# Kernel optimization log

Hardware: AMD Instinct MI355X
Metric: run time of the kernel (lower is better)

Reference implementation:

```python
import jax, jax.numpy as jnp
import numpy as np

B, S, E, H, D = 2, 2048, 768, 12, 64  # batch, seq, emb_dim, num_heads, encoder_emb_dim
EPS = 1e-5


def setup_inputs() -> dict:
    key = jax.random.key(0)
    ks = jax.random.split(key, 6)
    # kaiming-uniform-ish bound for fan_in=E
    bound = float(np.sqrt(6.0 / E))
    u = lambda k, shp: jax.random.uniform(k, shp, jnp.float32, -bound, bound)
    return {
        "x": jax.random.normal(ks[0], (B, S, E), jnp.float32),
        "ln_w": jnp.ones((E,), jnp.float32),
        "ln_b": jnp.zeros((E,), jnp.float32),
        "wq": u(ks[1], (E, H * D)),
        "bq": jnp.zeros((H * D,), jnp.float32),
        "wk": u(ks[2], (E, H * D)),
        "bk": jnp.zeros((H * D,), jnp.float32),
        "wv": u(ks[3], (E, H * D)),
        "bv": jnp.zeros((H * D,), jnp.float32),
        "wo": u(ks[4], (H * D, E)),
        "bo": jnp.zeros((E,), jnp.float32),
    }


def reference(x, ln_w, ln_b, wq, bq, wk, bk, wv, bv, wo, bo):
    b, s, _ = x.shape
    # LayerNorm (biased variance, eps=1e-5), as torch.nn.LayerNorm
    mu = x.mean(-1, keepdims=True)
    var = ((x - mu) ** 2).mean(-1, keepdims=True)
    xn = (x - mu) * jax.lax.rsqrt(var + EPS) * ln_w + ln_b

    q = (xn @ wq + bq).reshape(b, s, H, D)
    k = (xn @ wk + bk).reshape(b, s, H, D)
    v = (xn @ wv + bv).reshape(b, s, H, D)

    scale = 1.0 / np.sqrt(D).astype(np.float32)
    scores = jnp.einsum("bihd,bjhd->bhij", q, k) * scale  # [B,H,S,S]

    # masking=True, self_attending=True: mask STRICTLY lower triangle with -inf
    # (i.e. each position attends only to itself and FUTURE positions)
    mask = jnp.tril(jnp.ones((s, s), dtype=bool), k=-1)
    scores = jnp.where(mask, -jnp.inf, scores)

    a = jax.nn.softmax(scores, axis=-1)
    h = jnp.einsum("bhij,bjhd->bihd", a, v).reshape(b, s, H * D)
    return h @ wo + bo
```

## Files before the change

### kernel.cpp

```cpp
#include <hip/hip_runtime.h>

typedef __bf16 bf16_t;
typedef __bf16 bf16x8 __attribute__((ext_vector_type(8)));
typedef __bf16 bf16x4 __attribute__((ext_vector_type(4)));
typedef short  s16x4  __attribute__((ext_vector_type(4)));
typedef float  f32x4  __attribute__((ext_vector_type(4)));
typedef unsigned int u32;

#define BB 2
#define SS 2048
#define EE 768
#define HH 12
#define DD 64
#define NROW (BB*SS)

#define GLDS16(gp, lp) __builtin_amdgcn_global_load_lds( \
    (const __attribute__((address_space(1))) u32*)(gp),   \
    (__attribute__((address_space(3))) u32*)(lp), 16, 0, 0)

#if __has_builtin(__builtin_amdgcn_mfma_f32_16x16x16bf16_1k)
#define MFMA16_BUILTIN 1
static __device__ __forceinline__ f32x4 mfma_16x16x16_bf16(bf16x4 a, bf16x4 b, f32x4 c) {
  return __builtin_amdgcn_mfma_f32_16x16x16bf16_1k(
      __builtin_bit_cast(s16x4, a), __builtin_bit_cast(s16x4, b), c, 0, 0, 0);
}
#else
#define MFMA16_BUILTIN 0
static __device__ __forceinline__ f32x4 mfma_16x16x16_bf16(bf16x4 a, bf16x4 b, f32x4 c) {
  asm volatile("v_mfma_f32_16x16x16_bf16 %0, %1, %2, %0" : "+v"(c) : "v"(a), "v"(b));
  return c;
}
#endif

__global__ __launch_bounds__(256) void pack_w_kernel(
    const float* __restrict__ wq, const float* __restrict__ wk,
    const float* __restrict__ wv, const float* __restrict__ wo,
    bf16_t* __restrict__ wt)
{
  __shared__ float tile[64][65];
  const float* src = (blockIdx.z==0)?wq:(blockIdx.z==1)?wk:(blockIdx.z==2)?wv:wo;
  const int k0 = blockIdx.x*64, n0 = blockIdx.y*64;
  const int t = threadIdx.x;
  #pragma unroll
  for (int it=0; it<16; ++it) {
    int idx = it*256+t, r = idx>>6, c = idx&63;
    tile[r][c] = src[(size_t)(k0+r)*EE + n0 + c];
  }
  __syncthreads();
  bf16_t* dst = wt + (size_t)blockIdx.z*EE*EE;
  #pragma unroll
  for (int it=0; it<16; ++it) {
    int idx = it*256+t, r = idx>>6, c = idx&63;
    dst[(size_t)(n0+r)*EE + k0 + c] = (bf16_t)tile[c][r];
  }
}

__global__ __launch_bounds__(256) void ln_kernel(
    const float* __restrict__ x, const float* __restrict__ w,
    const float* __restrict__ bvec, bf16_t* __restrict__ xn)
{
  const int row = blockIdx.x, t = threadIdx.x;
  const float* xr = x + (size_t)row*EE;
  float v0 = xr[t], v1 = xr[t+256], v2 = xr[t+512];
  float s  = v0+v1+v2;
  float ss = v0*v0 + v1*v1 + v2*v2;
  #pragma unroll
  for (int m=1; m<64; m<<=1) { s += __shfl_xor(s,m); ss += __shfl_xor(ss,m); }
  __shared__ float red[2][4];
  const int wid = t>>6, lane = t&63;
  if (lane==0) { red[0][wid]=s; red[1][wid]=ss; }
  __syncthreads();
  s  = red[0][0]+red[0][1]+red[0][2]+red[0][3];
  ss = red[1][0]+red[1][1]+red[1][2]+red[1][3];
  const float mu   = s*(1.0f/EE);
  const float rstd = rsqrtf(ss*(1.0f/EE) - mu*mu + 1e-5f);
  bf16_t* xo = xn + (size_t)row*EE;
  xo[t      ] = (bf16_t)((v0-mu)*rstd*w[t      ] + bvec[t      ]);
  xo[t + 256] = (bf16_t)((v1-mu)*rstd*w[t + 256] + bvec[t + 256]);
  xo[t + 512] = (bf16_t)((v2-mu)*rstd*w[t + 512] + bvec[t + 512]);
}

__global__ __launch_bounds__(256) void gemm_qkv_kernel(
    const bf16_t* __restrict__ xn, const bf16_t* __restrict__ wt,
    const float* __restrict__ bq, const float* __restrict__ bk, const float* __restrict__ bv,
    bf16_t* __restrict__ qb, bf16_t* __restrict__ kb, bf16_t* __restrict__ vb)
{
  __shared__ __align__(16) bf16_t As[2][128][32];
  __shared__ __align__(16) bf16_t Bs[2][128][32];
  const int bm = blockIdx.x, by = blockIdx.y;
  const int mat = by/6, nb = by%6;
  const bf16_t* W = wt + (size_t)mat*EE*EE + (size_t)nb*128*EE;
  const float* bias = (mat==0)?bq:(mat==1)?bk:bv;
  bf16_t* outp = (mat==0)?qb:(mat==1)?kb:vb;
  const int t = threadIdx.x, lane = t&63, wid = t>>6;
  const int wr = wid>>1, wc = wid&1;
  const int lrow = lane&15, lk = lane>>4;
  const bf16_t* Ag = xn + (size_t)bm*128*EE;

  const int srow = t>>2, sp = t&3;
  const int sg = sp ^ ((srow>>1)&3);
  const int pcs = (lrow>>1)&3;

  auto stage = [&](int buf, int k0) {
    const bf16_t* asrc = Ag + (size_t)srow*EE + k0 + sg*8;
    const bf16_t* bsrc = W  + (size_t)srow*EE + k0 + sg*8;
    GLDS16(asrc,                 &As[buf][0][0] + t*8);
    GLDS16(asrc + (size_t)64*EE, &As[buf][0][0] + 2048 + t*8);
    GLDS16(bsrc,                 &Bs[buf][0][0] + t*8);
    GLDS16(bsrc + (size_t)64*EE, &Bs[buf][0][0] + 2048 + t*8);
  };

  f32x4 acc[4][4];
  #pragma unroll
  for (int i=0;i<4;++i)
    #pragma unroll
    for (int j=0;j<4;++j) acc[i][j] = (f32x4){0.f,0.f,0.f,0.f};

  stage(0, 0);
  __syncthreads();
  int cur = 0;
  for (int k0=0; k0<EE; k0+=32) {
    if (k0+32 < EE) stage(cur^1, k0+32);
    bf16x8 af[4], bfv[4];
    #pragma unroll
    for (int mi=0;mi<4;++mi) af[mi]  = *(const bf16x8*)&As[cur][wr*64+mi*16+lrow][(lk^pcs)*8];
    #pragma unroll
    for (int ni=0;ni<4;++ni) bfv[ni] = *(const bf16x8*)&Bs[cur][wc*64+ni*16+lrow][(lk^pcs)*8];
    #pragma unroll
    for (int mi=0;mi<4;++mi)
      #pragma unroll
      for (int ni=0;ni<4;++ni)
        acc[mi][ni] = __builtin_amdgcn_mfma_f32_16x16x32_bf16(af[mi], bfv[ni], acc[mi][ni], 0,0,0);
    __syncthreads();
    cur ^= 1;
  }
  const int m_base = bm*128 + wr*64;
  const int n_base = nb*128 + wc*64;
  #pragma unroll
  for (int ni=0;ni<4;++ni) {
    const int col = n_base + ni*16 + lrow;
    const float bias_v = bias[col];
    #pragma unroll
    for (int mi=0;mi<4;++mi) {
      #pragma unroll
      for (int r=0;r<4;++r) {
        int row = m_base + mi*16 + 4*lk + r;
        outp[(size_t)row*EE + col] = (bf16_t)(acc[mi][ni][r] + bias_v);
      }
    }
  }
}

__global__ __launch_bounds__(256) void vtrans_kernel(
    const bf16_t* __restrict__ v, bf16_t* __restrict__ vt)
{
  __shared__ __align__(16) bf16_t tile[64][72];
  const int j0 = blockIdx.x*64, bh = blockIdx.y;
  const int b = bh/HH, h = bh%HH;
  const int t = threadIdx.x;
  #pragma unroll
  for (int it=0; it<2; ++it) {
    int idx = it*256+t, r = idx>>3, c8 = (idx&7)*8;
    *(bf16x8*)&tile[r][c8] = *(const bf16x8*)(v + (size_t)(b*SS + j0 + r)*EE + h*DD + c8);
  }
  __syncthreads();
  #pragma unroll
  for (int it=0; it<2; ++it) {
    int idx = it*256+t, d = idx>>3, c8 = (idx&7)*8;
    bf16x8 val;
    #pragma unroll
    for (int i=0;i<8;++i) val[i] = tile[c8+i][d];
    *(bf16x8*)(vt + ((size_t)bh*DD + d)*SS + j0 + c8) = val;
  }
}

__global__ __launch_bounds__(256) void attn_kernel(
    const bf16_t* __restrict__ qb, const bf16_t* __restrict__ kb,
    const bf16_t* __restrict__ vt, bf16_t* __restrict__ hb)
{
  __shared__ __align__(16) bf16_t Ks[2][64][64];
  __shared__ __align__(16) bf16_t Vts[2][64][64];

  const int bid = blockIdx.x;
  const int rnd = bid >> 8, g = bid & 255;
  const int item = (rnd == 1) ? (511 - g) : (rnd*256 + g);
  const int qt = item / 24, bh = item % 24;

  const int i0 = qt*64, b = bh/HH, h = bh%HH;
  const int t = threadIdx.x, lane = t&63, wid = t>>6;
  const int lrow = lane&15, lk = lane>>4;

  const int srow = t>>3, sp = t&7;
  const int sgc = sp ^ (srow&7);
  const bf16_t* kbase  = kb + (size_t)b*SS*EE + h*DD;
  const bf16_t* vtbase = vt + (size_t)bh*DD*SS;

  const bf16_t* qrow = qb + (size_t)(b*SS + i0 + wid*16 + lrow)*EE + h*DD;
  const bf16x8 qf0 = *(const bf16x8*)(qrow + lk*8);
  const bf16x8 qf1 = *(const bf16x8*)(qrow + 32 + lk*8);

  f32x4 acc_ot[4];
  #pragma unroll
  for (int i=0;i<4;++i) acc_ot[i] = (f32x4){0.f,0.f,0.f,0.f};
  float lsum = 0.f;
  const int iloc = wid*16 + lrow;
  const int kkey = lrow&7;

  auto stage = [&](int buf, int jt) {
    const int j0v = jt*64;
    const bf16_t* ksrc = kbase  + (size_t)(j0v + srow)*EE + sgc*8;
    const bf16_t* vsrc = vtbase + (size_t)srow*SS + j0v + sgc*8;
    GLDS16(ksrc,                 &Ks[buf][0][0]  + t*8);
    GLDS16(ksrc + (size_t)32*EE, &Ks[buf][0][0]  + 2048 + t*8);
    GLDS16(vsrc,                 &Vts[buf][0][0] + t*8);
    GLDS16(vsrc + (size_t)32*SS, &Vts[buf][0][0] + 2048 + t*8);
  };

#define ATTN_TILE(CUR, MASKED) do {                                          \
    float e[4][4];                                                           \
    _Pragma("unroll")                                                        \
    for (int sj=0;sj<4;++sj) {                                               \
      const bf16_t* krow = &Ks[CUR][sj*16+lrow][0];                          \
      bf16x8 kf0 = *(const bf16x8*)(krow + ((lk^kkey)<<3));                  \
      bf16x8 kf1 = *(const bf16x8*)(krow + (((lk+4)^kkey)<<3));              \
      f32x4 a = (f32x4){0.f,0.f,0.f,0.f};                                    \
      a = __builtin_amdgcn_mfma_f32_16x16x32_bf16(kf0, qf0, a, 0,0,0);       \
      a = __builtin_amdgcn_mfma_f32_16x16x32_bf16(kf1, qf1, a, 0,0,0);       \
      _Pragma("unroll")                                                      \
      for (int r=0;r<4;++r) {                                                \
        float ee = a[r]*0.180336878f - 34.6246784f;                          \
        if (MASKED && (sj*16 + 4*lk + r) < iloc) ee = -1e30f;                \
        e[sj][r] = ee;                                                       \
      }                                                                      \
    }                                                                        \
    bf16x4 pb[4];                                                            \
    _Pragma("unroll")                                                        \
    for (int sj=0;sj<4;++sj)                                                 \
      _Pragma("unroll")                                                      \
      for (int r=0;r<4;++r) {                                                \
        float p = exp2f(e[sj][r]);                                           \
        lsum += p;                                                           \
        pb[sj][r] = (bf16_t)p;                                               \
      }                                                                      \
    _Pragma("unroll")                                                        \
    for (int sd=0;sd<4;++sd) {                                               \
      const bf16_t* vrow = &Vts[CUR][sd*16+lrow][0];                         \
      _Pragma("unroll")                                                      \
      for (int sj=0;sj<4;++sj) {                                             \
        bf16x4 vf = *(const bf16x4*)(vrow + (((2*sj+(lk>>1))^kkey)<<3) + ((lk&1)<<2)); \
        acc_ot[sd] = mfma_16x16x16_bf16(vf, pb[sj], acc_ot[sd]);             \
      }                                                                      \
    }                                                                        \
  } while(0)

  const int ntiles = SS/64 - qt;
  stage(0, qt);
  __syncthreads();
  if (ntiles > 1) stage(1, qt+1);
  ATTN_TILE(0, true);
#if !MFMA16_BUILTIN
  asm volatile("s_nop 7\n\ts_nop 7");
#endif
  __syncthreads();

  int cur = 1;
  for (int it2=1; it2<ntiles; ++it2) {
    if (it2+1 < ntiles) stage(cur^1, qt+it2+1);
    ATTN_TILE(cur, false);
#if !MFMA16_BUILTIN
    asm volatile("s_nop 7\n\ts_nop 7");
#endif
    __syncthreads();
    cur ^= 1;
  }
#undef ATTN_TILE

  lsum += __shfl_xor(lsum, 16);
  lsum += __shfl_xor(lsum, 32);
  const float inv = 1.0f / lsum;

  const int erow = wid*16 + lrow, ekey = erow&7;
  #pragma unroll
  for (int sd=0;sd<4;++sd) {
    bf16x4 ov;
    #pragma unroll
    for (int r=0;r<4;++r) ov[r] = (bf16_t)(acc_ot[sd][r] * inv);
    *(bf16x4*)(&Ks[0][erow][0] + (((2*sd+(lk>>1))^ekey)<<3) + ((lk&1)<<2)) = ov;
  }
  __syncthreads();
  const int rq = wid*16 + (lane>>2), rkey = rq&7, c4 = lane&3;
  bf16x8 o0 = *(const bf16x8*)(&Ks[0][rq][0] + (((2*c4  )^rkey)<<3));
  bf16x8 o1 = *(const bf16x8*)(&Ks[0][rq][0] + (((2*c4+1)^rkey)<<3));
  bf16_t* orow = hb + (size_t)(b*SS + i0 + rq)*EE + h*DD + c4*16;
  *(bf16x8*)orow = o0;
  *(bf16x8*)(orow+8) = o1;
}

__global__ __launch_bounds__(256) void gemm_out_kernel(
    const bf16_t* __restrict__ hbuf, const bf16_t* __restrict__ wto,
    const float* __restrict__ bo, float* __restrict__ out)
{
  __shared__ __align__(16) bf16_t As[2][128][32];
  __shared__ __align__(16) bf16_t Bs[2][128][32];
  const int bm = blockIdx.x, nb = blockIdx.y;
  const bf16_t* W = wto + (size_t)nb*128*EE;
  const int t = threadIdx.x, lane = t&63, wid = t>>6;
  const int wr = wid>>1, wc = wid&1;
  const int lrow = lane&15, lk = lane>>4;
  const bf16_t* Ag = hbuf + (size_t)bm*128*EE;

  const int srow = t>>2, sp = t&3;
  const int sg = sp ^ ((srow>>1)&3);
  const int pcs = (lrow>>1)&3;

  auto stage = [&](int buf, int k0) {
    const bf16_t* asrc = Ag + (size_t)srow*EE + k0 + sg*8;
    const bf16_t* bsrc = W  + (size_t)srow*EE + k0 + sg*8;
    GLDS16(asrc,                 &As[buf][0][0] + t*8);
    GLDS16(asrc + (size_t)64*EE, &As[buf][0][0] + 2048 + t*8);
    GLDS16(bsrc,                 &Bs[buf][0][0] + t*8);
    GLDS16(bsrc + (size_t)64*EE, &Bs[buf][0][0] + 2048 + t*8);
  };

  f32x4 acc[4][4];
  #pragma unroll
  for (int i=0;i<4;++i)
    #pragma unroll
    for (int j=0;j<4;++j) acc[i][j] = (f32x4){0.f,0.f,0.f,0.f};

  stage(0, 0);
  __syncthreads();
  int cur = 0;
  for (int k0=0; k0<EE; k0+=32) {
    if (k0+32 < EE) stage(cur^1, k0+32);
    bf16x8 af[4], bfv[4];
    #pragma unroll
    for (int mi=0;mi<4;++mi) af[mi]  = *(const bf16x8*)&As[cur][wr*64+mi*16+lrow][(lk^pcs)*8];
    #pragma unroll
    for (int ni=0;ni<4;++ni) bfv[ni] = *(const bf16x8*)&Bs[cur][wc*64+ni*16+lrow][(lk^pcs)*8];
    #pragma unroll
    for (int mi=0;mi<4;++mi)
      #pragma unroll
      for (int ni=0;ni<4;++ni)
        acc[mi][ni] = __builtin_amdgcn_mfma_f32_16x16x32_bf16(af[mi], bfv[ni], acc[mi][ni], 0,0,0);
    __syncthreads();
    cur ^= 1;
  }
  const int m_base = bm*128 + wr*64;
  const int n_base = nb*128 + wc*64;
  #pragma unroll
  for (int ni=0;ni<4;++ni) {
    const int col = n_base + ni*16 + lrow;
    const float bias_v = bo[col];
    #pragma unroll
    for (int mi=0;mi<4;++mi) {
      #pragma unroll
      for (int r=0;r<4;++r) {
        int row = m_base + mi*16 + 4*lk + r;
        out[(size_t)row*EE + col] = acc[mi][ni][r] + bias_v;
      }
    }
  }
}

extern "C" void kernel_launch(void* const* d_in, const int* in_sizes, int n_in,
                              void* d_out, int out_size, void* d_ws, size_t ws_size,
                              hipStream_t stream) {
  const float* x    = (const float*)d_in[0];
  const float* ln_w = (const float*)d_in[1];
  const float* ln_b = (const float*)d_in[2];
  const float* wq   = (const float*)d_in[3];
  const float* bq   = (const float*)d_in[4];
  const float* wk   = (const float*)d_in[5];
  const float* bk   = (const float*)d_in[6];
  const float* wv   = (const float*)d_in[7];
  const float* bv   = (const float*)d_in[8];
  const float* wo   = (const float*)d_in[9];
  const float* bo   = (const float*)d_in[10];
  float* out = (float*)d_out;

  char* ws = (char*)d_ws;
  bf16_t* wt  = (bf16_t*)(ws);
  bf16_t* xn  = (bf16_t*)(ws + 4718592);
  bf16_t* qb  = (bf16_t*)(ws + 11010048);
  bf16_t* kb  = (bf16_t*)(ws + 17301504);
  bf16_t* vb  = (bf16_t*)(ws + 23592960);
  bf16_t* vtb = (bf16_t*)(ws + 29884416);
  bf16_t* hb  = (bf16_t*)(ws + 36175872);

  pack_w_kernel  <<<dim3(12,12,4), 256, 0, stream>>>(wq, wk, wv, wo, wt);
  ln_kernel      <<<dim3(NROW),    256, 0, stream>>>(x, ln_w, ln_b, xn);
  gemm_qkv_kernel<<<dim3(32,18),   256, 0, stream>>>(xn, wt, bq, bk, bv, qb, kb, vb);
  vtrans_kernel  <<<dim3(32,24),   256, 0, stream>>>(vb, vtb);
  attn_kernel    <<<dim3(768),     256, 0, stream>>>(qb, kb, vtb, hb);
  gemm_out_kernel<<<dim3(32,6),    256, 0, stream>>>(hb, wt + (size_t)3*EE*EE, bo, out);
}
```

Measured before the change: 95.58 us.

## Split attention KV range into segments with a separate combine kernel

The attention grid is split along the key dimension. Long query tiles get 2 or 3 segments, giving 1512 blocks instead of 768 with better-balanced work per block. Partial unnormalized outputs and row sums go to fp32 workspace, and a new combine kernel sums and normalizes them. This relies on the softmax not subtracting a running max, so partial sums can simply be added. The cost is an extra kernel launch and fp32 partial-result traffic.

```diff
diff --git a/kernel.cpp b/kernel.cpp
--- a/kernel.cpp
+++ b/kernel.cpp
@@ -176,15 +176,23 @@
 
 __global__ __launch_bounds__(256) void attn_kernel(
     const bf16_t* __restrict__ qb, const bf16_t* __restrict__ kb,
-    const bf16_t* __restrict__ vt, bf16_t* __restrict__ hb)
+    const bf16_t* __restrict__ vt, bf16_t* __restrict__ hb,
+    float* __restrict__ pO, float* __restrict__ pl)
 {
   __shared__ __align__(16) bf16_t Ks[2][64][64];
   __shared__ __align__(16) bf16_t Vts[2][64][64];
 
-  const int bid = blockIdx.x;
-  const int rnd = bid >> 8, g = bid & 255;
-  const int item = (rnd == 1) ? (511 - g) : (rnd*256 + g);
-  const int qt = item / 24, bh = item % 24;
+  const int w = blockIdx.x;
+  const int bh = w / 63, s = w % 63;
+  int qt, seg;
+  if (s < 30)      { qt = s/3;           seg = s%3;       }
+  else if (s < 52) { qt = 10 + (s-30)/2; seg = (s-30)&1;  }
+  else             { qt = 21 + (s-52);   seg = 0;         }
+  const int L = 32 - qt;
+  const int nseg = (qt<10) ? 3 : (qt<21) ? 2 : 1;
+  const int base = L/nseg, rem = L%nseg;
+  const int jt0 = qt + seg*base + (seg<rem ? seg : rem);
+  const int len = base + (seg<rem ? 1 : 0);
 
   const int i0 = qt*64, b = bh/HH, h = bh%HH;
   const int t = threadIdx.x, lane = t&63, wid = t>>6;
@@ -253,19 +261,18 @@
     }                                                                        \
   } while(0)
 
-  const int ntiles = SS/64 - qt;
-  stage(0, qt);
-  __syncthreads();
-  if (ntiles > 1) stage(1, qt+1);
-  ATTN_TILE(0, true);
+  stage(0, jt0);
+  __syncthreads();
+  if (len > 1) stage(1, jt0+1);
+  if (seg == 0) { ATTN_TILE(0, true); } else { ATTN_TILE(0, false); }
 #if !MFMA16_BUILTIN
   asm volatile("s_nop 7\n\ts_nop 7");
 #endif
   __syncthreads();
 
   int cur = 1;
-  for (int it2=1; it2<ntiles; ++it2) {
-    if (it2+1 < ntiles) stage(cur^1, qt+it2+1);
+  for (int it2=1; it2<len; ++it2) {
+    if (it2+1 < len) stage(cur^1, jt0+it2+1);
     ATTN_TILE(cur, false);
 #if !MFMA16_BUILTIN
     asm volatile("s_nop 7\n\ts_nop 7");
@@ -277,8 +284,18 @@
 
   lsum += __shfl_xor(lsum, 16);
   lsum += __shfl_xor(lsum, 32);
+
+  if (nseg > 1) {
+    const size_t slot = ((size_t)qt*24 + bh)*3 + seg;
+    float* po = pO + slot*4096 + (size_t)(wid*16 + lrow)*64;
+    #pragma unroll
+    for (int sd=0;sd<4;++sd)
+      *(f32x4*)(po + sd*16 + 4*lk) = acc_ot[sd];
+    if (lane < 16) pl[slot*64 + wid*16 + lrow] = lsum;
+    return;
+  }
+
   const float inv = 1.0f / lsum;
-
   const int erow = wid*16 + lrow, ekey = erow&7;
   #pragma unroll
   for (int sd=0;sd<4;++sd) {
@@ -294,6 +311,40 @@
   bf16_t* orow = hb + (size_t)(b*SS + i0 + rq)*EE + h*DD + c4*16;
   *(bf16x8*)orow = o0;
   *(bf16x8*)(orow+8) = o1;
+}
+
+__global__ __launch_bounds__(256) void attn_combine_kernel(
+    const float* __restrict__ pO, const float* __restrict__ pl,
+    bf16_t* __restrict__ hb)
+{
+  const int qt = blockIdx.x;
+  const int bh = blockIdx.y;
+  const int nseg = (qt < 10) ? 3 : 2;
+  const int t = threadIdx.x;
+  const int q = t >> 2, d0 = (t & 3) * 16;
+  const size_t slot = ((size_t)qt*24 + bh)*3;
+
+  float l = pl[slot*64 + q] + pl[(slot+1)*64 + q];
+  if (nseg == 3) l += pl[(slot+2)*64 + q];
+  const float inv = 1.0f / l;
+
+  const float* o0 = pO + (slot  )*4096 + (size_t)q*64 + d0;
+  const float* o1 = pO + (slot+1)*4096 + (size_t)q*64 + d0;
+  const float* o2 = pO + (slot+2)*4096 + (size_t)q*64 + d0;
+  const int b = bh/HH, h = bh%HH;
+  bf16_t* orow = hb + (size_t)(b*SS + qt*64 + q)*EE + h*DD + d0;
+
+  #pragma unroll
+  for (int c=0;c<4;++c) {
+    f32x4 v = *(const f32x4*)(o0 + c*4);
+    f32x4 v1 = *(const f32x4*)(o1 + c*4);
+    v += v1;
+    if (nseg == 3) { f32x4 v2 = *(const f32x4*)(o2 + c*4); v += v2; }
+    bf16x4 ov;
+    #pragma unroll
+    for (int i=0;i<4;++i) ov[i] = (bf16_t)(v[i]*inv);
+    *(bf16x4*)(orow + c*4) = ov;
+  }
 }
 
 __global__ __launch_bounds__(256) void gemm_out_kernel(
@@ -387,11 +438,14 @@
   bf16_t* vb  = (bf16_t*)(ws + 23592960);
   bf16_t* vtb = (bf16_t*)(ws + 29884416);
   bf16_t* hb  = (bf16_t*)(ws + 36175872);
+  float*  pO  = (float*)(ws + 42467328);
+  float*  pl  = (float*)(ws + 80216064);
 
   pack_w_kernel  <<<dim3(12,12,4), 256, 0, stream>>>(wq, wk, wv, wo, wt);
   ln_kernel      <<<dim3(NROW),    256, 0, stream>>>(x, ln_w, ln_b, xn);
   gemm_qkv_kernel<<<dim3(32,18),   256, 0, stream>>>(xn, wt, bq, bk, bv, qb, kb, vb);
   vtrans_kernel  <<<dim3(32,24),   256, 0, stream>>>(vb, vtb);
-  attn_kernel    <<<dim3(768),     256, 0, stream>>>(qb, kb, vtb, hb);
+  attn_kernel    <<<dim3(1512),    256, 0, stream>>>(qb, kb, vtb, hb, pO, pl);
+  attn_combine_kernel<<<dim3(21,24), 256, 0, stream>>>(pO, pl, hb);
   gemm_out_kernel<<<dim3(32,6),    256, 0, stream>>>(hb, wt + (size_t)3*EE*EE, bo, out);
 }
```

Result: slower. 102.5 us (+7.2%).

## Triple-buffer LDS staging with vmcnt-based waits and one barrier per step

Applied to the files above, without the earlier changes.

Moves the QKV GEMM, output GEMM and attention kernels from double to triple-buffered LDS staging. Each step now prefetches two tiles ahead, waits with s_waitcnt vmcnt(4) so only the current tile's loads must land, and uses a single barrier per iteration instead of two. The aim is to hide global-load latency and cut barrier stalls, at the cost of more LDS per block (possible occupancy loss) and reliance on exact vmcnt accounting of the async global_load_lds ops.

```diff
diff --git a/kernel.cpp b/kernel.cpp
--- a/kernel.cpp
+++ b/kernel.cpp
@@ -17,6 +17,13 @@
 #define GLDS16(gp, lp) __builtin_amdgcn_global_load_lds( \
     (const __attribute__((address_space(1))) u32*)(gp),   \
     (__attribute__((address_space(3))) u32*)(lp), 16, 0, 0)
+
+static __device__ __forceinline__ void pipe_wait(bool more_in_flight) {
+  if (more_in_flight) asm volatile("s_waitcnt vmcnt(4)" ::: "memory");
+  else                asm volatile("s_waitcnt vmcnt(0)" ::: "memory");
+  __builtin_amdgcn_s_barrier();
+  asm volatile("" ::: "memory");
+}
 
 #if __has_builtin(__builtin_amdgcn_mfma_f32_16x16x16bf16_1k)
 #define MFMA16_BUILTIN 1
@@ -85,8 +92,8 @@
     const float* __restrict__ bq, const float* __restrict__ bk, const float* __restrict__ bv,
     bf16_t* __restrict__ qb, bf16_t* __restrict__ kb, bf16_t* __restrict__ vb)
 {
-  __shared__ __align__(16) bf16_t As[2][128][32];
-  __shared__ __align__(16) bf16_t Bs[2][128][32];
+  __shared__ __align__(16) bf16_t As[3][128][32];
+  __shared__ __align__(16) bf16_t Bs[3][128][32];
   const int bm = blockIdx.x, by = blockIdx.y;
   const int mat = by/6, nb = by%6;
   const bf16_t* W = wt + (size_t)mat*EE*EE + (size_t)nb*128*EE;
@@ -116,23 +123,27 @@
     #pragma unroll
     for (int j=0;j<4;++j) acc[i][j] = (f32x4){0.f,0.f,0.f,0.f};
 
+  const int NK = EE/32;
   stage(0, 0);
-  __syncthreads();
-  int cur = 0;
-  for (int k0=0; k0<EE; k0+=32) {
-    if (k0+32 < EE) stage(cur^1, k0+32);
+  stage(1, 32);
+  int bufi = 0;
+  for (int ks=0; ks<NK; ++ks) {
+    pipe_wait(ks+1 < NK);
+    if (ks+2 < NK) {
+      int nb2 = (bufi >= 1) ? bufi-1 : 2;
+      stage(nb2, (ks+2)*32);
+    }
     bf16x8 af[4], bfv[4];
     #pragma unroll
-    for (int mi=0;mi<4;++mi) af[mi]  = *(const bf16x8*)&As[cur][wr*64+mi*16+lrow][(lk^pcs)*8];
-    #pragma unroll
-    for (int ni=0;ni<4;++ni) bfv[ni] = *(const bf16x8*)&Bs[cur][wc*64+ni*16+lrow][(lk^pcs)*8];
+    for (int mi=0;mi<4;++mi) af[mi]  = *(const bf16x8*)&As[bufi][wr*64+mi*16+lrow][(lk^pcs)*8];
+    #pragma unroll
+    for (int ni=0;ni<4;++ni) bfv[ni] = *(const bf16x8*)&Bs[bufi][wc*64+ni*16+lrow][(lk^pcs)*8];
     #pragma unroll
     for (int mi=0;mi<4;++mi)
       #pragma unroll
       for (int ni=0;ni<4;++ni)
         acc[mi][ni] = __builtin_amdgcn_mfma_f32_16x16x32_bf16(af[mi], bfv[ni], acc[mi][ni], 0,0,0);
-    __syncthreads();
-    cur ^= 1;
+    bufi = (bufi==2) ? 0 : bufi+1;
   }
   const int m_base = bm*128 + wr*64;
   const int n_base = nb*128 + wc*64;
@@ -178,8 +189,8 @@
     const bf16_t* __restrict__ qb, const bf16_t* __restrict__ kb,
     const bf16_t* __restrict__ vt, bf16_t* __restrict__ hb)
 {
-  __shared__ __align__(16) bf16_t Ks[2][64][64];
-  __shared__ __align__(16) bf16_t Vts[2][64][64];
+  __shared__ __align__(16) bf16_t Ks[3][64][64];
+  __shared__ __align__(16) bf16_t Vts[3][64][64];
 
   const int bid = blockIdx.x;
   const int rnd = bid >> 8, g = bid & 255;
@@ -216,11 +227,11 @@
     GLDS16(vsrc + (size_t)32*SS, &Vts[buf][0][0] + 2048 + t*8);
   };
 
-#define ATTN_TILE(CUR, MASKED) do {                                          \
+#define ATTN_TILE(KB, VB, MASKED) do {                                       \
     float e[4][4];                                                           \
     _Pragma("unroll")                                                        \
     for (int sj=0;sj<4;++sj) {                                               \
-      const bf16_t* krow = &Ks[CUR][sj*16+lrow][0];                          \
+      const bf16_t* krow = (KB) + (sj*16+lrow)*64;                           \
       bf16x8 kf0 = *(const bf16x8*)(krow + ((lk^kkey)<<3));                  \
       bf16x8 kf1 = *(const bf16x8*)(krow + (((lk+4)^kkey)<<3));              \
       f32x4 a = (f32x4){0.f,0.f,0.f,0.f};                                    \
@@ -244,7 +255,7 @@
       }                                                                      \
     _Pragma("unroll")                                                        \
     for (int sd=0;sd<4;++sd) {                                               \
-      const bf16_t* vrow = &Vts[CUR][sd*16+lrow][0];                         \
+      const bf16_t* vrow = (VB) + (sd*16+lrow)*64;                           \
       _Pragma("unroll")                                                      \
       for (int sj=0;sj<4;++sj) {                                             \
         bf16x4 vf = *(const bf16x4*)(vrow + (((2*sj+(lk>>1))^kkey)<<3) + ((lk&1)<<2)); \
@@ -255,23 +266,27 @@
 
   const int ntiles = SS/64 - qt;
   stage(0, qt);
-  __syncthreads();
   if (ntiles > 1) stage(1, qt+1);
-  ATTN_TILE(0, true);
+
+  pipe_wait(ntiles > 1);
+  if (2 < ntiles) stage(2, qt+2);
+  ATTN_TILE(&Ks[0][0][0], &Vts[0][0][0], true);
 #if !MFMA16_BUILTIN
   asm volatile("s_nop 7\n\ts_nop 7");
 #endif
-  __syncthreads();
-
-  int cur = 1;
+
+  int bufi = 1;
   for (int it2=1; it2<ntiles; ++it2) {
-    if (it2+1 < ntiles) stage(cur^1, qt+it2+1);
-    ATTN_TILE(cur, false);
+    pipe_wait(it2+1 < ntiles);
+    if (it2+2 < ntiles) {
+      int nb2 = (bufi >= 1) ? bufi-1 : 2;
+      stage(nb2, qt+it2+2);
+    }
+    ATTN_TILE(&Ks[bufi][0][0], &Vts[bufi][0][0], false);
 #if !MFMA16_BUILTIN
     asm volatile("s_nop 7\n\ts_nop 7");
 #endif
-    __syncthreads();
-    cur ^= 1;
+    bufi = (bufi==2) ? 0 : bufi+1;
   }
 #undef ATTN_TILE
 
@@ -279,6 +294,7 @@
   lsum += __shfl_xor(lsum, 32);
   const float inv = 1.0f / lsum;
 
+  __syncthreads();
   const int erow = wid*16 + lrow, ekey = erow&7;
   #pragma unroll
   for (int sd=0;sd<4;++sd) {
@@ -300,8 +316,8 @@
     const bf16_t* __restrict__ hbuf, const bf16_t* __restrict__ wto,
     const float* __restrict__ bo, float* __restrict__ out)
 {
-  __shared__ __align__(16) bf16_t As[2][128][32];
-  __shared__ __align__(16) bf16_t Bs[2][128][32];
+  __shared__ __align__(16) bf16_t As[3][128][32];
+  __shared__ __align__(16) bf16_t Bs[3][128][32];
   const int bm = blockIdx.x, nb = blockIdx.y;
   const bf16_t* W = wto + (size_t)nb*128*EE;
   const int t = threadIdx.x, lane = t&63, wid = t>>6;
@@ -328,23 +344,27 @@
     #pragma unroll
     for (int j=0;j<4;++j) acc[i][j] = (f32x4){0.f,0.f,0.f,0.f};
 
+  const int NK = EE/32;
   stage(0, 0);
-  __syncthreads();
-  int cur = 0;
-  for (int k0=0; k0<EE; k0+=32) {
-    if (k0+32 < EE) stage(cur^1, k0+32);
+  stage(1, 32);
+  int bufi = 0;
+  for (int ks=0; ks<NK; ++ks) {
+    pipe_wait(ks+1 < NK);
+    if (ks+2 < NK) {
+      int nb2 = (bufi >= 1) ? bufi-1 : 2;
+      stage(nb2, (ks+2)*32);
+    }
     bf16x8 af[4], bfv[4];
     #pragma unroll
-    for (int mi=0;mi<4;++mi) af[mi]  = *(const bf16x8*)&As[cur][wr*64+mi*16+lrow][(lk^pcs)*8];
-    #pragma unroll
-    for (int ni=0;ni<4;++ni) bfv[ni] = *(const bf16x8*)&Bs[cur][wc*64+ni*16+lrow][(lk^pcs)*8];
+    for (int mi=0;mi<4;++mi) af[mi]  = *(const bf16x8*)&As[bufi][wr*64+mi*16+lrow][(lk^pcs)*8];
+    #pragma unroll
+    for (int ni=0;ni<4;++ni) bfv[ni] = *(const bf16x8*)&Bs[bufi][wc*64+ni*16+lrow][(lk^pcs)*8];
     #pragma unroll
     for (int mi=0;mi<4;++mi)
       #pragma unroll
       for (int ni=0;ni<4;++ni)
         acc[mi][ni] = __builtin_amdgcn_mfma_f32_16x16x32_bf16(af[mi], bfv[ni], acc[mi][ni], 0,0,0);
-    __syncthreads();
-    cur ^= 1;
+    bufi = (bufi==2) ? 0 : bufi+1;
   }
   const int m_base = bm*128 + wr*64;
   const int n_base = nb*128 + wc*64;
```

Result: slower. 102.3 us (+7.1%).

## Load attention K/V fragments directly from global into registers, dropping LDS staging

Applied to the files above, without the earlier changes.

The attention kernel no longer stages K and V^T tiles into double-buffered shared memory with async global-to-LDS copies and barriers. Each wave now loads its own K and V fragments straight from global memory into registers every tile and fuses the exp step into the score loop. It also sets launch bounds to 3 blocks per CU and uses a small padded LDS buffer only for the output transpose. This removes LDS traffic and per-tile __syncthreads, but the four waves in a block now each fetch the same K/V data from global/L2 with no cross-wave reuse, and memory latency is exposed with no explicit prefetch.

```diff
diff --git a/kernel.cpp b/kernel.cpp
--- a/kernel.cpp
+++ b/kernel.cpp
@@ -174,13 +174,10 @@
   }
 }
 
-__global__ __launch_bounds__(256) void attn_kernel(
+__global__ __launch_bounds__(256, 3) void attn_kernel(
     const bf16_t* __restrict__ qb, const bf16_t* __restrict__ kb,
     const bf16_t* __restrict__ vt, bf16_t* __restrict__ hb)
 {
-  __shared__ __align__(16) bf16_t Ks[2][64][64];
-  __shared__ __align__(16) bf16_t Vts[2][64][64];
-
   const int bid = blockIdx.x;
   const int rnd = bid >> 8, g = bid & 255;
   const int item = (rnd == 1) ? (511 - g) : (rnd*256 + g);
@@ -190,8 +187,6 @@
   const int t = threadIdx.x, lane = t&63, wid = t>>6;
   const int lrow = lane&15, lk = lane>>4;
 
-  const int srow = t>>3, sp = t&7;
-  const int sgc = sp ^ (srow&7);
   const bf16_t* kbase  = kb + (size_t)b*SS*EE + h*DD;
   const bf16_t* vtbase = vt + (size_t)bh*DD*SS;
 
@@ -204,74 +199,59 @@
   for (int i=0;i<4;++i) acc_ot[i] = (f32x4){0.f,0.f,0.f,0.f};
   float lsum = 0.f;
   const int iloc = wid*16 + lrow;
-  const int kkey = lrow&7;
-
-  auto stage = [&](int buf, int jt) {
-    const int j0v = jt*64;
-    const bf16_t* ksrc = kbase  + (size_t)(j0v + srow)*EE + sgc*8;
-    const bf16_t* vsrc = vtbase + (size_t)srow*SS + j0v + sgc*8;
-    GLDS16(ksrc,                 &Ks[buf][0][0]  + t*8);
-    GLDS16(ksrc + (size_t)32*EE, &Ks[buf][0][0]  + 2048 + t*8);
-    GLDS16(vsrc,                 &Vts[buf][0][0] + t*8);
-    GLDS16(vsrc + (size_t)32*SS, &Vts[buf][0][0] + 2048 + t*8);
-  };
-
-#define ATTN_TILE(CUR, MASKED) do {                                          \
-    float e[4][4];                                                           \
+
+  const bf16_t* kp = kbase + (size_t)(qt*64 + lrow)*EE + lk*8;
+  const bf16_t* vp = vtbase + (size_t)lrow*SS + qt*64 + 4*lk;
+
+#define ATTN_TILE(MASKED) do {                                               \
+    bf16x8 kf[4][2];                                                         \
     _Pragma("unroll")                                                        \
     for (int sj=0;sj<4;++sj) {                                               \
-      const bf16_t* krow = &Ks[CUR][sj*16+lrow][0];                          \
-      bf16x8 kf0 = *(const bf16x8*)(krow + ((lk^kkey)<<3));                  \
-      bf16x8 kf1 = *(const bf16x8*)(krow + (((lk+4)^kkey)<<3));              \
+      const bf16_t* kr = kp + (size_t)(sj*16)*EE;                            \
+      kf[sj][0] = *(const bf16x8*)kr;                                        \
+      kf[sj][1] = *(const bf16x8*)(kr + 32);                                 \
+    }                                                                        \
+    bf16x4 vf[4][4];                                                         \
+    _Pragma("unroll")                                                        \
+    for (int sd=0;sd<4;++sd) {                                               \
+      const bf16_t* vr = vp + (size_t)(sd*16)*SS;                            \
+      _Pragma("unroll")                                                      \
+      for (int sj=0;sj<4;++sj) vf[sd][sj] = *(const bf16x4*)(vr + sj*16);    \
+    }                                                                        \
+    bf16x4 pb[4];                                                            \
+    _Pragma("unroll")                                                        \
+    for (int sj=0;sj<4;++sj) {                                               \
       f32x4 a = (f32x4){0.f,0.f,0.f,0.f};                                    \
-      a = __builtin_amdgcn_mfma_f32_16x16x32_bf16(kf0, qf0, a, 0,0,0);       \
-      a = __builtin_amdgcn_mfma_f32_16x16x32_bf16(kf1, qf1, a, 0,0,0);       \
+      a = __builtin_amdgcn_mfma_f32_16x16x32_bf16(kf[sj][0], qf0, a, 0,0,0); \
+      a = __builtin_amdgcn_mfma_f32_16x16x32_bf16(kf[sj][1], qf1, a, 0,0,0); \
       _Pragma("unroll")                                                      \
       for (int r=0;r<4;++r) {                                                \
         float ee = a[r]*0.180336878f - 34.6246784f;                          \
         if (MASKED && (sj*16 + 4*lk + r) < iloc) ee = -1e30f;                \
-        e[sj][r] = ee;                                                       \
-      }                                                                      \
-    }                                                                        \
-    bf16x4 pb[4];                                                            \
-    _Pragma("unroll")                                                        \
-    for (int sj=0;sj<4;++sj)                                                 \
-      _Pragma("unroll")                                                      \
-      for (int r=0;r<4;++r) {                                                \
-        float p = exp2f(e[sj][r]);                                           \
+        float p = exp2f(ee);                                                 \
         lsum += p;                                                           \
         pb[sj][r] = (bf16_t)p;                                               \
       }                                                                      \
+    }                                                                        \
     _Pragma("unroll")                                                        \
-    for (int sd=0;sd<4;++sd) {                                               \
-      const bf16_t* vrow = &Vts[CUR][sd*16+lrow][0];                         \
+    for (int sd=0;sd<4;++sd)                                                 \
       _Pragma("unroll")                                                      \
-      for (int sj=0;sj<4;++sj) {                                             \
-        bf16x4 vf = *(const bf16x4*)(vrow + (((2*sj+(lk>>1))^kkey)<<3) + ((lk&1)<<2)); \
-        acc_ot[sd] = mfma_16x16x16_bf16(vf, pb[sj], acc_ot[sd]);             \
-      }                                                                      \
-    }                                                                        \
+      for (int sj=0;sj<4;++sj)                                               \
+        acc_ot[sd] = mfma_16x16x16_bf16(vf[sd][sj], pb[sj], acc_ot[sd]);     \
   } while(0)
 
-  const int ntiles = SS/64 - qt;
-  stage(0, qt);
-  __syncthreads();
-  if (ntiles > 1) stage(1, qt+1);
-  ATTN_TILE(0, true);
+  ATTN_TILE(true);
+  kp += (size_t)64*EE; vp += 64;
 #if !MFMA16_BUILTIN
   asm volatile("s_nop 7\n\ts_nop 7");
 #endif
-  __syncthreads();
-
-  int cur = 1;
-  for (int it2=1; it2<ntiles; ++it2) {
-    if (it2+1 < ntiles) stage(cur^1, qt+it2+1);
-    ATTN_TILE(cur, false);
+
+  for (int jt=qt+1; jt<SS/64; ++jt) {
+    ATTN_TILE(false);
+    kp += (size_t)64*EE; vp += 64;
 #if !MFMA16_BUILTIN
     asm volatile("s_nop 7\n\ts_nop 7");
 #endif
-    __syncthreads();
-    cur ^= 1;
   }
 #undef ATTN_TILE
 
@@ -279,18 +259,19 @@
   lsum += __shfl_xor(lsum, 32);
   const float inv = 1.0f / lsum;
 
-  const int erow = wid*16 + lrow, ekey = erow&7;
+  __shared__ __align__(16) bf16_t Os[64][72];
+  const int erow = wid*16 + lrow;
   #pragma unroll
   for (int sd=0;sd<4;++sd) {
     bf16x4 ov;
     #pragma unroll
     for (int r=0;r<4;++r) ov[r] = (bf16_t)(acc_ot[sd][r] * inv);
-    *(bf16x4*)(&Ks[0][erow][0] + (((2*sd+(lk>>1))^ekey)<<3) + ((lk&1)<<2)) = ov;
-  }
-  __syncthreads();
-  const int rq = wid*16 + (lane>>2), rkey = rq&7, c4 = lane&3;
-  bf16x8 o0 = *(const bf16x8*)(&Ks[0][rq][0] + (((2*c4  )^rkey)<<3));
-  bf16x8 o1 = *(const bf16x8*)(&Ks[0][rq][0] + (((2*c4+1)^rkey)<<3));
+    *(bf16x4*)&Os[erow][sd*16 + 4*lk] = ov;
+  }
+  __syncthreads();
+  const int rq = wid*16 + (lane>>2), c4 = lane&3;
+  bf16x8 o0 = *(const bf16x8*)&Os[rq][c4*16];
+  bf16x8 o1 = *(const bf16x8*)&Os[rq][c4*16 + 8];
   bf16_t* orow = hb + (size_t)(b*SS + i0 + rq)*EE + h*DD + c4*16;
   *(bf16x8*)orow = o0;
   *(bf16x8*)(orow+8) = o1;
```

Measured after the change: 202.4 us. +111.7%, slower.
